# Kernel optimization log

Hardware: AMD Instinct MI355X
Metric: run time of the kernel (lower is better)

## Reference

```python
import jax, jax.numpy as jnp
import numpy as np

N = 50000
E = 800000
F_IN = 128
HID = 16
HEADS = 8
CLS = 16
NEG_SLOPE = 0.2


def setup_inputs() -> dict:
    key = jax.random.key(0)
    ks = jax.random.split(key, 12)
    x = jax.random.normal(ks[0], (N, F_IN), dtype=jnp.float32)
    edge_index = jax.random.randint(ks[1], (2, E), 0, N, dtype=jnp.int32)
    s = 0.1
    W1 = jax.random.normal(ks[2], (F_IN, HEADS * HID), dtype=jnp.float32) * s
    att_src1 = jax.random.normal(ks[3], (HEADS, HID), dtype=jnp.float32) * s
    att_dst1 = jax.random.normal(ks[4], (HEADS, HID), dtype=jnp.float32) * s
    b1 = jax.random.normal(ks[5], (HEADS * HID,), dtype=jnp.float32) * s
    W2 = jax.random.normal(ks[6], (HEADS * HID, CLS), dtype=jnp.float32) * s
    att_src2 = jax.random.normal(ks[7], (1, CLS), dtype=jnp.float32) * s
    att_dst2 = jax.random.normal(ks[8], (1, CLS), dtype=jnp.float32) * s
    b2 = jax.random.normal(ks[9], (CLS,), dtype=jnp.float32) * s
    return {"x": x, "edge_index": edge_index, "W1": W1, "att_src1": att_src1,
            "att_dst1": att_dst1, "b1": b1, "W2": W2, "att_src2": att_src2,
            "att_dst2": att_dst2, "b2": b2}


def _gat_conv(x, src, dst, W, a_src, a_dst, b, heads, out_ch, concat):
    n = x.shape[0]
    h = (x @ W).reshape(n, heads, out_ch)                     # [N,H,C]
    alpha_src = (h * a_src[None]).sum(-1)                     # [N,H]
    alpha_dst = (h * a_dst[None]).sum(-1)                     # [N,H]
    e = jax.nn.leaky_relu(alpha_src[src] + alpha_dst[dst], NEG_SLOPE)  # [E,H]
    m = jax.lax.stop_gradient(jax.ops.segment_max(e, dst, num_segments=n))
    e = jnp.exp(e - m[dst])
    denom = jax.ops.segment_sum(e, dst, num_segments=n)
    alpha = e / (denom[dst] + 1e-16)                          # [E,H]
    msg = h[src] * alpha[:, :, None]                          # [E,H,C]
    out = jax.ops.segment_sum(msg, dst, num_segments=n)       # [N,H,C]
    out = out.reshape(n, heads * out_ch) if concat else out.mean(axis=1)
    return out + b


def reference(x, edge_index, W1, att_src1, att_dst1, b1, W2, att_src2, att_dst2, b2):
    # PyG GATConv default add_self_loops=True
    loop = jnp.arange(N, dtype=edge_index.dtype)
    src = jnp.concatenate([edge_index[0], loop])
    dst = jnp.concatenate([edge_index[1], loop])
    h = _gat_conv(x, src, dst, W1, att_src1, att_dst1, b1, HEADS, HID, True)
    h = jax.nn.elu(h)
    # dropout inactive (eval mode)
    out = _gat_conv(h, src, dst, W2, att_src2, att_dst2, b2, 1, CLS, False)
    return out
```

## Files before the change

### kernel.cpp

```cpp
#include <hip/hip_runtime.h>
#include <hip/hip_bf16.h>
#include <limits.h>
#include <math.h>

#define N 50000
#define E_ 800000
#define ETOT 850000
#define HH 128
#define HEADS 8
#define HID 16
#define CLS 16
#define NEG 0.2f
#define NB ((N + 255) / 256)
#define GBM 64
#define GEMM_NB ((N + GBM - 1) / GBM)
#define LINK_NB ((ETOT + 255) / 256)
#define PREP_NB ((128*128 + 255) / 256)
#define A1_NB ((N*HEADS + 255) / 256)

typedef unsigned short u16;
typedef unsigned int   u32;
typedef short s8v __attribute__((ext_vector_type(8)));
typedef float f4v __attribute__((ext_vector_type(4)));

__device__ __forceinline__ u16 f2bu(float f){
  union{float f; u32 i;} c; c.f = f;
  u32 lsb = (c.i >> 16) & 1u;
  c.i += 0x7fffu + lsb;
  return (u16)(c.i >> 16);
}
__device__ __forceinline__ float bu2f(u16 u){
  union{u32 i; float f;} c; c.i = ((u32)u) << 16; return c.f;
}
__device__ __forceinline__ float blo(u32 u){ union{u32 i; float f;} c; c.i = u << 16; return c.f; }
__device__ __forceinline__ float bhi(u32 u){ union{u32 i; float f;} c; c.i = u & 0xffff0000u; return c.f; }

__global__ __launch_bounds__(256) void k_init(int* __restrict__ head){
  int i = blockIdx.x*256 + threadIdx.x;
  if(i < N) head[i] = -1;
}

__global__ __launch_bounds__(256) void k_linkprep(const int* __restrict__ ei,
                                                  int* __restrict__ head,
                                                  int* __restrict__ srcv,
                                                  int* __restrict__ nxt,
                                                  const float* __restrict__ W1,
                                                  const float* __restrict__ W2,
                                                  u16* __restrict__ wth, u16* __restrict__ wtl,
                                                  u16* __restrict__ w2th, u16* __restrict__ w2tl){
  if(blockIdx.x < PREP_NB){
    int i = blockIdx.x*256 + threadIdx.x;
    if(i < 128*128){
      int k = i >> 7, c = i & 127;
      float v = W1[i];
      u16 hi = f2bu(v);
      wth[c*128 + k] = hi;
      wtl[c*128 + k] = f2bu(v - bu2f(hi));
    }
    if(i < 128*16){
      int k = i >> 4, c = i & 15;
      float v = W2[i];
      u16 hi = f2bu(v);
      w2th[c*128 + k] = hi;
      w2tl[c*128 + k] = f2bu(v - bu2f(hi));
    }
    return;
  }
  int e = (blockIdx.x - PREP_NB)*256 + threadIdx.x;
  if(e >= ETOT) return;
  int s, d;
  if(e < E_){ s = ei[e]; d = ei[E_ + e]; } else { s = d = e - E_; }
  int old = atomicExch(&head[d], e);
  srcv[e] = s;
  nxt[e]  = old;
}

__global__ __launch_bounds__(256) void k_gemm1walk(const float* __restrict__ x,
                                                   const u16* __restrict__ wth,
                                                   const u16* __restrict__ wtl,
                                                   u16* __restrict__ h1b,
                                                   const int* __restrict__ head,
                                                   const int* __restrict__ nxt,
                                                   int* __restrict__ deg,
                                                   int* __restrict__ bsum){
  __shared__ u16 xh[GBM][40], xl[GBM][40];
  __shared__ u16 wh[128][40], wl[128][40];
  __shared__ int sm[256];
  if(blockIdx.x >= GEMM_NB){
    int b = blockIdx.x - GEMM_NB;
    int t = threadIdx.x;
    int i = b*256 + t;
    int cnt = 0;
    if(i < N){
      int e = head[i];
      while(e >= 0){ cnt++; e = nxt[e]; }
      deg[i] = cnt;
    }
    sm[t] = cnt;
    __syncthreads();
    #pragma unroll
    for(int ofs=128; ofs>0; ofs>>=1){
      if(t < ofs) sm[t] += sm[t+ofs];
      __syncthreads();
    }
    if(t == 0) bsum[b] = sm[0];
    return;
  }
  int tid  = threadIdx.x;
  int wv   = tid >> 6;
  int lane = tid & 63;
  int row0 = blockIdx.x * GBM;

  f4v acc[4][2];
  #pragma unroll
  for(int t=0;t<4;t++)
    #pragma unroll
    for(int u=0;u<2;u++) acc[t][u] = (f4v){0.f,0.f,0.f,0.f};

  int xr  = tid >> 2;
  int xkq = (tid & 3) * 8;
  int wc  = tid & 127;
  int wq  = (tid >> 7) * 8;
  int xrow = row0 + xr; if(xrow >= N) xrow = N-1;
  const float* xb = x + (size_t)xrow*128 + xkq;
  int fr = lane & 15, fg = lane >> 4;
  int kk = fg*8;

  for(int kc=0; kc<4; kc++){
    int k0 = kc*32;
    float4 v0 = *(const float4*)(xb + k0);
    float4 v1 = *(const float4*)(xb + k0 + 4);
    __syncthreads();
    {
      float vv[8] = {v0.x,v0.y,v0.z,v0.w,v1.x,v1.y,v1.z,v1.w};
      s8v H, L;
      #pragma unroll
      for(int j=0;j<8;j++){
        u16 h_ = f2bu(vv[j]);
        H[j] = (short)h_;
        L[j] = (short)f2bu(vv[j] - bu2f(h_));
      }
      *(s8v*)&xh[xr][xkq] = H;
      *(s8v*)&xl[xr][xkq] = L;
    }
    #pragma unroll
    for(int j=0;j<2;j++){
      int kq = wq + j*16;
      *(s8v*)&wh[wc][kq] = *(const s8v*)&wth[wc*128 + k0 + kq];
      *(s8v*)&wl[wc][kq] = *(const s8v*)&wtl[wc*128 + k0 + kq];
    }
    __syncthreads();
    s8v a_h[4], a_l[4], b_h[2], b_l[2];
    #pragma unroll
    for(int t=0;t<4;t++){
      a_h[t] = *(const s8v*)&xh[t*16 + fr][kk];
      a_l[t] = *(const s8v*)&xl[t*16 + fr][kk];
    }
    #pragma unroll
    for(int u=0;u<2;u++){
      int col = wv*32 + u*16 + fr;
      b_h[u] = *(const s8v*)&wh[col][kk];
      b_l[u] = *(const s8v*)&wl[col][kk];
    }
    #pragma unroll
    for(int t=0;t<4;t++){
      #pragma unroll
      for(int u=0;u<2;u++){
        acc[t][u] = __builtin_amdgcn_mfma_f32_16x16x32_bf16(a_h[t], b_h[u], acc[t][u], 0,0,0);
        acc[t][u] = __builtin_amdgcn_mfma_f32_16x16x32_bf16(a_h[t], b_l[u], acc[t][u], 0,0,0);
        acc[t][u] = __builtin_amdgcn_mfma_f32_16x16x32_bf16(a_l[t], b_h[u], acc[t][u], 0,0,0);
      }
    }
  }
  #pragma unroll
  for(int t=0;t<4;t++){
    #pragma unroll
    for(int j=0;j<4;j++){
      int row = row0 + t*16 + fg*4 + j;
      if(row < N){
        u16* dst = h1b + (size_t)row*128 + wv*32 + fr;
        dst[0]  = f2bu(acc[t][0][j]);
        dst[16] = f2bu(acc[t][1][j]);
      }
    }
  }
}

__global__ __launch_bounds__(256) void k_scan3alpha(const int* __restrict__ deg,
                                                    const int* __restrict__ bsum,
                                                    const int* __restrict__ head,
                                                    const int* __restrict__ srcv,
                                                    const int* __restrict__ nxt,
                                                    int* __restrict__ off,
                                                    int* __restrict__ csr,
                                                    const u16* __restrict__ h1b,
                                                    const float* __restrict__ Asv,
                                                    const float* __restrict__ Adv,
                                                    float* __restrict__ as1,
                                                    float* __restrict__ ad1){
  __shared__ int red[256];
  __shared__ int sm[256];
  if(blockIdx.x < NB){
    int t = threadIdx.x;
    red[t] = (t < blockIdx.x) ? bsum[t] : 0;
    __syncthreads();
    #pragma unroll
    for(int ofs=128; ofs>0; ofs>>=1){
      if(t < ofs) red[t] += red[t+ofs];
      __syncthreads();
    }
    int boff = red[0];
    int i = blockIdx.x*256 + t;
    int v0 = (i < N) ? deg[i] : 0;
    sm[t] = v0;
    __syncthreads();
    #pragma unroll
    for(int ofs=1; ofs<256; ofs<<=1){
      int v = sm[t];
      int add = (t >= ofs) ? sm[t-ofs] : 0;
      __syncthreads();
      sm[t] = v + add;
      __syncthreads();
    }
    if(i < N){
      int excl = boff + sm[t] - v0;
      off[i] = excl;
      if(i == N-1) off[N] = excl + v0;
      int e = head[i];
      int pos = excl;
      while(e >= 0){
        csr[pos++] = srcv[e];
        e = nxt[e];
      }
    }
    return;
  }
  int id = (blockIdx.x - NB)*256 + threadIdx.x;
  if(id >= N*HEADS) return;
  int i = id >> 3, h = id & 7;
  const uint4* hv = (const uint4*)(h1b + (size_t)i*HH + h*HID);
  uint4 u0 = hv[0], u1 = hv[1];
  float vals[16] = {blo(u0.x),bhi(u0.x),blo(u0.y),bhi(u0.y),
                    blo(u0.z),bhi(u0.z),blo(u0.w),bhi(u0.w),
                    blo(u1.x),bhi(u1.x),blo(u1.y),bhi(u1.y),
                    blo(u1.z),bhi(u1.z),blo(u1.w),bhi(u1.w)};
  float s=0.f, d=0.f;
  #pragma unroll
  for(int j=0;j<16;j++){
    s = fmaf(vals[j], Asv[h*HID+j], s);
    d = fmaf(vals[j], Adv[h*HID+j], d);
  }
  as1[id]=s; ad1[id]=d;
}

#define CH 32
__global__ __launch_bounds__(256) void k_agg1(const int* __restrict__ off,
                                              const int* __restrict__ csr,
                                              const float* __restrict__ as1,
                                              const float* __restrict__ ad1,
                                              const u32* __restrict__ h1w,
                                              const float* __restrict__ b1,
                                              u32* __restrict__ helu_w){
  __shared__ float wsm[4][CH*8];
  __shared__ int   ssm[4][CH];
  int wv   = threadIdx.x >> 6;
  int lane = threadIdx.x & 63;
  int node = blockIdx.x*4 + wv;
  int beg = off[node], end = off[node+1];
  int h  = lane >> 3;
  int hh = lane & 7;
  int el = lane >> 3;
  float advA = ad1[node*8 + hh];
  float den = 0.f, num0 = 0.f, num1 = 0.f;
  float* wsw = wsm[wv];
  int*   ssw = ssm[wv];
  const u32* hp = h1w + lane;
  for(int base = beg; base < end; base += CH){
    int cnt = end - base; if(cnt > CH) cnt = CH;
    #pragma unroll
    for(int k=0;k<CH;k+=8){
      int e = el + k;
      if(e < cnt){
        int s = csr[base+e];
        if(hh == 0) ssw[e] = s;
        float v = as1[s*8+hh] + advA;
        v = v > 0.f ? v : NEG*v;
        wsw[e*8+hh] = __expf(v);
      }
    }
    int e = 0;
    for(; e+8 <= cnt; e += 8){
      int ss[8]; float ww[8]; u32 uu[8];
      #pragma unroll
      for(int j=0;j<8;j++){ ss[j] = ssw[e+j]; ww[j] = wsw[(e+j)*8+h]; }
      #pragma unroll
      for(int j=0;j<8;j++){ uu[j] = hp[(size_t)ss[j]*64]; }
      #pragma unroll
      for(int j=0;j<8;j++){
        den += ww[j];
        num0 = fmaf(ww[j], blo(uu[j]), num0);
        num1 = fmaf(ww[j], bhi(uu[j]), num1);
      }
    }
    for(; e+4 <= cnt; e += 4){
      int ss[4]; float ww[4]; u32 uu[4];
      #pragma unroll
      for(int j=0;j<4;j++){ ss[j] = ssw[e+j]; ww[j] = wsw[(e+j)*8+h]; }
      #pragma unroll
      for(int j=0;j<4;j++){ uu[j] = hp[(size_t)ss[j]*64]; }
      #pragma unroll
      for(int j=0;j<4;j++){
        den += ww[j];
        num0 = fmaf(ww[j], blo(uu[j]), num0);
        num1 = fmaf(ww[j], bhi(uu[j]), num1);
      }
    }
    for(; e < cnt; e++){
      int s = ssw[e];
      float w = wsw[e*8+h];
      u32 u = hp[(size_t)s*64];
      den += w;
      num0 = fmaf(w, blo(u), num0);
      num1 = fmaf(w, bhi(u), num1);
    }
  }
  float2 bb = ((const float2*)b1)[lane];
  float inv = 1.f / (den + 1e-16f);
  float r0 = num0*inv + bb.x;
  float r1 = num1*inv + bb.y;
  r0 = r0 > 0.f ? r0 : expm1f(r0);
  r1 = r1 > 0.f ? r1 : expm1f(r1);
  helu_w[(size_t)node*64 + lane] = (u32)f2bu(r0) | ((u32)f2bu(r1) << 16);
}

__global__ __launch_bounds__(256) void k_gemm2m(const u16* __restrict__ helu,
                                                const u16* __restrict__ w2th,
                                                const u16* __restrict__ w2tl,
                                                const float* __restrict__ Asv,
                                                const float* __restrict__ Adv,
                                                u16* __restrict__ h2b,
                                                float* __restrict__ as2,
                                                float* __restrict__ ad2){
  __shared__ u16 At[4][16][136];
  __shared__ u16 Bh[16][136], Bl[16][136];
  int tid  = threadIdx.x;
  int wv   = tid >> 6;
  int lane = tid & 63;
  int fr = lane & 15, fg = lane >> 4;
  int row0 = blockIdx.x*64 + wv*16;

  {
    int r = tid >> 4, c8 = (tid & 15)*8;
    *(s8v*)&Bh[r][c8] = *(const s8v*)&w2th[r*128 + c8];
    *(s8v*)&Bl[r][c8] = *(const s8v*)&w2tl[r*128 + c8];
  }
  #pragma unroll
  for(int j=0;j<4;j++){
    int rl = j*4 + (lane >> 4);
    int rg = row0 + rl; if(rg >= N) rg = N-1;
    *(s8v*)&At[wv][rl][(lane & 15)*8] = *(const s8v*)&helu[(size_t)rg*128 + (lane & 15)*8];
  }
  __syncthreads();

  f4v acc = (f4v){0.f,0.f,0.f,0.f};
  #pragma unroll
  for(int kc=0; kc<4; kc++){
    int kk = kc*32 + fg*8;
    s8v a  = *(const s8v*)&At[wv][fr][kk];
    s8v bh = *(const s8v*)&Bh[fr][kk];
    s8v bl = *(const s8v*)&Bl[fr][kk];
    acc = __builtin_amdgcn_mfma_f32_16x16x32_bf16(a, bh, acc, 0,0,0);
    acc = __builtin_amdgcn_mfma_f32_16x16x32_bf16(a, bl, acc, 0,0,0);
  }
  float asv = Asv[fr], adv = Adv[fr];
  #pragma unroll
  for(int j=0;j<4;j++){
    int row = row0 + fg*4 + j;
    float ps = acc[j]*asv, pd = acc[j]*adv;
    ps += __shfl_xor(ps,1); ps += __shfl_xor(ps,2); ps += __shfl_xor(ps,4); ps += __shfl_xor(ps,8);
    pd += __shfl_xor(pd,1); pd += __shfl_xor(pd,2); pd += __shfl_xor(pd,4); pd += __shfl_xor(pd,8);
    if(row < N){
      h2b[(size_t)row*16 + fr] = f2bu(acc[j]);
      if(fr == 0){ as2[row] = ps; ad2[row] = pd; }
    }
  }
}

__global__ __launch_bounds__(256) void k_agg2(const int* __restrict__ off,
                                              const int* __restrict__ csr,
                                              const float* __restrict__ as2,
                                              const float* __restrict__ ad2,
                                              const u32* __restrict__ h2w,
                                              const float* __restrict__ b2,
                                              float* __restrict__ outp){
  int t = threadIdx.x;
  int node = blockIdx.x*32 + (t >> 3);
  int c2 = t & 7;
  if(node >= N) return;
  int beg = off[node], end = off[node+1];
  float adv = ad2[node];
  float den = 0.f, num0 = 0.f, num1 = 0.f;
  int gbase = t & 56;
  for(int base = beg; base < end; base += 8){
    int cnt = end - base; if(cnt > 8) cnt = 8;
    float w_my = 0.f; int s_my = 0;
    if(c2 < cnt){
      s_my = csr[base + c2];
      float v = as2[s_my] + adv;
      v = v > 0.f ? v : NEG*v;
      w_my = __expf(v);
    }
    float ww[8]; int ss[8]; u32 uu[8];
    #pragma unroll
    for(int j=0;j<8;j++){
      ww[j] = __shfl(w_my, gbase | j);
      ss[j] = __shfl(s_my, gbase | j);
    }
    #pragma unroll
    for(int j=0;j<8;j++){
      if(j < cnt) uu[j] = h2w[(size_t)ss[j]*8 + c2];
    }
    #pragma unroll
    for(int j=0;j<8;j++){
      if(j < cnt){
        den += ww[j];
        num0 = fmaf(ww[j], blo(uu[j]), num0);
        num1 = fmaf(ww[j], bhi(uu[j]), num1);
      }
    }
  }
  float inv = 1.f / (den + 1e-16f);
  float2 bb = ((const float2*)b2)[c2];
  float2 r;
  r.x = num0*inv + bb.x;
  r.y = num1*inv + bb.y;
  ((float2*)outp)[(size_t)node*8 + c2] = r;
}

extern "C" void kernel_launch(void* const* d_in, const int* in_sizes, int n_in,
                              void* d_out, int out_size, void* d_ws, size_t ws_size,
                              hipStream_t stream){
  const float* x     = (const float*)d_in[0];
  const int*   ei    = (const int*)  d_in[1];
  const float* W1    = (const float*)d_in[2];
  const float* av_s1 = (const float*)d_in[3];
  const float* av_d1 = (const float*)d_in[4];
  const float* b1    = (const float*)d_in[5];
  const float* W2    = (const float*)d_in[6];
  const float* av_s2 = (const float*)d_in[7];
  const float* av_d2 = (const float*)d_in[8];
  const float* b2    = (const float*)d_in[9];
  float* outp = (float*)d_out;

  char* p = (char*)d_ws;
  auto alloc = [&](size_t bytes){ char* q = p; p += (bytes + 255) & ~(size_t)255; return q; };
  u16*   h1b    = (u16*)  alloc((size_t)N*HH*2);
  u16*   helu_b = (u16*)  alloc((size_t)N*HH*2);
  u16*   h2b    = (u16*)  alloc((size_t)N*CLS*2);
  float* as1    = (float*)alloc((size_t)N*HEADS*4);
  float* ad1    = (float*)alloc((size_t)N*HEADS*4);
  float* as2    = (float*)alloc((size_t)N*4);
  float* ad2    = (float*)alloc((size_t)N*4);
  int*   deg    = (int*)  alloc((size_t)N*4);
  int*   head   = (int*)  alloc((size_t)N*4);
  int*   off    = (int*)  alloc((size_t)(N+1)*4);
  int*   csr    = (int*)  alloc((size_t)ETOT*4);
  int*   srcv   = (int*)  alloc((size_t)ETOT*4);
  int*   nxt    = (int*)  alloc((size_t)ETOT*4);
  u16*   wth    = (u16*)  alloc((size_t)128*128*2);
  u16*   wtl    = (u16*)  alloc((size_t)128*128*2);
  u16*   w2th   = (u16*)  alloc((size_t)16*128*2);
  u16*   w2tl   = (u16*)  alloc((size_t)16*128*2);
  int*   bsum   = (int*)  alloc((size_t)NB*4);

  k_init<<<NB, 256, 0, stream>>>(head);

  k_linkprep<<<PREP_NB + LINK_NB, 256, 0, stream>>>(ei, head, srcv, nxt,
                                                    W1, W2, wth, wtl, w2th, w2tl);

  k_gemm1walk<<<GEMM_NB + NB, 256, 0, stream>>>(x, wth, wtl, h1b, head, nxt, deg, bsum);

  k_scan3alpha<<<NB + A1_NB, 256, 0, stream>>>(deg, bsum, head, srcv, nxt, off, csr,
                                               h1b, av_s1, av_d1, as1, ad1);

  k_agg1<<<N/4, 256, 0, stream>>>(off, csr, as1, ad1, (const u32*)h1b, b1, (u32*)helu_b);

  k_gemm2m<<<(N+63)/64, 256, 0, stream>>>(helu_b, w2th, w2tl, av_s2, av_d2, h2b, as2, ad2);
  k_agg2<<<(N+31)/32, 256, 0, stream>>>(off, csr, as2, ad2, (const u32*)h2b, b2, outp);
}
```

Measured before the change: 149.0 us.

## Split layer-1 features into head-pair planes and aggregate per plane

```diff
diff --git a/kernel.cpp b/kernel.cpp
--- a/kernel.cpp
+++ b/kernel.cpp
@@ -17,6 +17,8 @@
 #define LINK_NB ((ETOT + 255) / 256)
 #define PREP_NB ((128*128 + 255) / 256)
 #define A1_NB ((N*HEADS + 255) / 256)
+#define AGG1_NPB 4
+#define AGG1_PB (N / (AGG1_NPB))
 
 typedef unsigned short u16;
 typedef unsigned int   u32;
@@ -78,7 +80,7 @@
 __global__ __launch_bounds__(256) void k_gemm1walk(const float* __restrict__ x,
                                                    const u16* __restrict__ wth,
                                                    const u16* __restrict__ wtl,
-                                                   u16* __restrict__ h1b,
+                                                   u16* __restrict__ h1hm,
                                                    const int* __restrict__ head,
                                                    const int* __restrict__ nxt,
                                                    int* __restrict__ deg,
@@ -178,9 +180,10 @@
     for(int j=0;j<4;j++){
       int row = row0 + t*16 + fg*4 + j;
       if(row < N){
-        u16* dst = h1b + (size_t)row*128 + wv*32 + fr;
-        dst[0]  = f2bu(acc[t][0][j]);
-        dst[16] = f2bu(acc[t][1][j]);
+        int c0 = wv*32 + fr;
+        u16* d0 = h1hm + (size_t)((c0>>5)*N + row)*32 + (c0&31);
+        d0[0]  = f2bu(acc[t][0][j]);
+        d0[16] = f2bu(acc[t][1][j]);
       }
     }
   }
@@ -193,7 +196,7 @@
                                                     const int* __restrict__ nxt,
                                                     int* __restrict__ off,
                                                     int* __restrict__ csr,
-                                                    const u16* __restrict__ h1b,
+                                                    const u16* __restrict__ h1hm,
                                                     const float* __restrict__ Asv,
                                                     const float* __restrict__ Adv,
                                                     float* __restrict__ as1,
@@ -238,7 +241,7 @@
   int id = (blockIdx.x - NB)*256 + threadIdx.x;
   if(id >= N*HEADS) return;
   int i = id >> 3, h = id & 7;
-  const uint4* hv = (const uint4*)(h1b + (size_t)i*HH + h*HID);
+  const uint4* hv = (const uint4*)(h1hm + (size_t)((h>>1)*N + i)*32 + (h&1)*16);
   uint4 u0 = hv[0], u1 = hv[1];
   float vals[16] = {blo(u0.x),bhi(u0.x),blo(u0.y),bhi(u0.y),
                     blo(u0.z),bhi(u0.z),blo(u0.w),bhi(u0.w),
@@ -250,7 +253,8 @@
     s = fmaf(vals[j], Asv[h*HID+j], s);
     d = fmaf(vals[j], Adv[h*HID+j], d);
   }
-  as1[id]=s; ad1[id]=d;
+  as1[(size_t)h*N + i] = s;
+  ad1[(size_t)h*N + i] = d;
 }
 
 #define CH 32
@@ -261,76 +265,70 @@
                                               const u32* __restrict__ h1w,
                                               const float* __restrict__ b1,
                                               u32* __restrict__ helu_w){
-  __shared__ float wsm[4][CH*8];
+  __shared__ float wsm[4][CH*2];
   __shared__ int   ssm[4][CH];
+  int p    = blockIdx.x / AGG1_PB;
+  int blk  = blockIdx.x % AGG1_PB;
   int wv   = threadIdx.x >> 6;
   int lane = threadIdx.x & 63;
-  int node = blockIdx.x*4 + wv;
+  int node = blk*4 + wv;
   int beg = off[node], end = off[node+1];
-  int h  = lane >> 3;
-  int hh = lane & 7;
-  int el = lane >> 3;
-  float advA = ad1[node*8 + hh];
+  int ea  = lane & 31;
+  int hh2 = lane >> 5;
+  int headA = 2*p + hh2;
+  int cq = lane & 15;
+  int eq = lane >> 4;
+  int hsel = cq >> 3;
+  float advA = ad1[(size_t)headA*N + node];
   float den = 0.f, num0 = 0.f, num1 = 0.f;
   float* wsw = wsm[wv];
   int*   ssw = ssm[wv];
-  const u32* hp = h1w + lane;
+  const u32* hp = h1w + (size_t)p*N*16;
+  const float* asp = as1 + (size_t)headA*N;
   for(int base = beg; base < end; base += CH){
     int cnt = end - base; if(cnt > CH) cnt = CH;
-    #pragma unroll
-    for(int k=0;k<CH;k+=8){
-      int e = el + k;
-      if(e < cnt){
-        int s = csr[base+e];
-        if(hh == 0) ssw[e] = s;
-        float v = as1[s*8+hh] + advA;
-        v = v > 0.f ? v : NEG*v;
-        wsw[e*8+hh] = __expf(v);
-      }
-    }
-    int e = 0;
-    for(; e+8 <= cnt; e += 8){
-      int ss[8]; float ww[8]; u32 uu[8];
-      #pragma unroll
-      for(int j=0;j<8;j++){ ss[j] = ssw[e+j]; ww[j] = wsw[(e+j)*8+h]; }
-      #pragma unroll
-      for(int j=0;j<8;j++){ uu[j] = hp[(size_t)ss[j]*64]; }
-      #pragma unroll
-      for(int j=0;j<8;j++){
-        den += ww[j];
-        num0 = fmaf(ww[j], blo(uu[j]), num0);
-        num1 = fmaf(ww[j], bhi(uu[j]), num1);
-      }
-    }
-    for(; e+4 <= cnt; e += 4){
-      int ss[4]; float ww[4]; u32 uu[4];
-      #pragma unroll
-      for(int j=0;j<4;j++){ ss[j] = ssw[e+j]; ww[j] = wsw[(e+j)*8+h]; }
-      #pragma unroll
-      for(int j=0;j<4;j++){ uu[j] = hp[(size_t)ss[j]*64]; }
-      #pragma unroll
-      for(int j=0;j<4;j++){
-        den += ww[j];
-        num0 = fmaf(ww[j], blo(uu[j]), num0);
-        num1 = fmaf(ww[j], bhi(uu[j]), num1);
-      }
-    }
-    for(; e < cnt; e++){
-      int s = ssw[e];
-      float w = wsw[e*8+h];
-      u32 u = hp[(size_t)s*64];
-      den += w;
-      num0 = fmaf(w, blo(u), num0);
-      num1 = fmaf(w, bhi(u), num1);
-    }
-  }
-  float2 bb = ((const float2*)b1)[lane];
-  float inv = 1.f / (den + 1e-16f);
-  float r0 = num0*inv + bb.x;
-  float r1 = num1*inv + bb.y;
-  r0 = r0 > 0.f ? r0 : expm1f(r0);
-  r1 = r1 > 0.f ? r1 : expm1f(r1);
-  helu_w[(size_t)node*64 + lane] = (u32)f2bu(r0) | ((u32)f2bu(r1) << 16);
+    if(ea < cnt){
+      int s = csr[base+ea];
+      if(hh2 == 0) ssw[ea] = s;
+      float v = asp[s] + advA;
+      v = v > 0.f ? v : NEG*v;
+      wsw[ea*2+hh2] = __expf(v);
+    }
+    int q = 0;
+    for(; q+8 <= cnt; q += 8){
+      int qa = q+eq, qb = q+4+eq;
+      int sa = ssw[qa], sb = ssw[qb];
+      float wa = wsw[qa*2+hsel], wb = wsw[qb*2+hsel];
+      u32 ua = hp[(size_t)sa*16 + cq];
+      u32 ub = hp[(size_t)sb*16 + cq];
+      den += wa + wb;
+      num0 = fmaf(wa, blo(ua), num0); num1 = fmaf(wa, bhi(ua), num1);
+      num0 = fmaf(wb, blo(ub), num0); num1 = fmaf(wb, bhi(ub), num1);
+    }
+    for(; q < cnt; q += 4){
+      int qa = q + eq;
+      if(qa < cnt){
+        int sa = ssw[qa];
+        float wa = wsw[qa*2+hsel];
+        u32 ua = hp[(size_t)sa*16 + cq];
+        den += wa;
+        num0 = fmaf(wa, blo(ua), num0);
+        num1 = fmaf(wa, bhi(ua), num1);
+      }
+    }
+  }
+  num0 += __shfl_xor(num0,16); num0 += __shfl_xor(num0,32);
+  num1 += __shfl_xor(num1,16); num1 += __shfl_xor(num1,32);
+  den  += __shfl_xor(den,16);  den  += __shfl_xor(den,32);
+  if(eq == 0){
+    float2 bb = ((const float2*)b1)[p*16 + cq];
+    float inv = 1.f / (den + 1e-16f);
+    float r0 = num0*inv + bb.x;
+    float r1 = num1*inv + bb.y;
+    r0 = r0 > 0.f ? r0 : expm1f(r0);
+    r1 = r1 > 0.f ? r1 : expm1f(r1);
+    helu_w[(size_t)(p*N + node)*16 + cq] = (u32)f2bu(r0) | ((u32)f2bu(r1) << 16);
+  }
 }
 
 __global__ __launch_bounds__(256) void k_gemm2m(const u16* __restrict__ helu,
@@ -358,7 +356,8 @@
   for(int j=0;j<4;j++){
     int rl = j*4 + (lane >> 4);
     int rg = row0 + rl; if(rg >= N) rg = N-1;
-    *(s8v*)&At[wv][rl][(lane & 15)*8] = *(const s8v*)&helu[(size_t)rg*128 + (lane & 15)*8];
+    int c0 = (lane & 15)*8;
+    *(s8v*)&At[wv][rl][c0] = *(const s8v*)&helu[(size_t)((c0>>5)*N + rg)*32 + (c0&31)];
   }
   __syncthreads();
 
@@ -483,7 +482,7 @@
   k_scan3alpha<<<NB + A1_NB, 256, 0, stream>>>(deg, bsum, head, srcv, nxt, off, csr,
                                                h1b, av_s1, av_d1, as1, ad1);
 
-  k_agg1<<<N/4, 256, 0, stream>>>(off, csr, as1, ad1, (const u32*)h1b, b1, (u32*)helu_b);
+  k_agg1<<<4*AGG1_PB, 256, 0, stream>>>(off, csr, as1, ad1, (const u32*)h1b, b1, (u32*)helu_b);
 
   k_gemm2m<<<(N+63)/64, 256, 0, stream>>>(helu_b, w2th, w2tl, av_s2, av_d2, h2b, as2, ad2);
   k_agg2<<<(N+31)/32, 256, 0, stream>>>(off, csr, as2, ad2, (const u32*)h2b, b2, outp);
```

After: 193.5 us. +29.8%, slower.
